# Optimization experiments

Hardware: AMD Instinct MI355X
Metric: run time of the kernel (lower is better)

Reference implementation:

```python
import jax, jax.numpy as jnp
import numpy as np

HEAD = 16
FEAT = 32
OUT = 32
N_E = 2048
N_UP = 1024  # n_up init kwarg (closed over; determines up/down split of x)


def _eps_ksi():
    # Complex-multiplication structure tensors (sparse 2x2x2), as in the source.
    ksi = (jnp.zeros((2, 2, 2))
           .at[0, 0, 0].set(1.0).at[1, 1, 0].set(-1.0)
           .at[0, 1, 1].set(1.0).at[1, 0, 1].set(1.0))
    eps = (jnp.zeros((2, 2, 2))
           .at[0, 0, 0].set(1.0).at[1, 1, 0].set(1.0)
           .at[0, 1, 1].set(1.0).at[1, 0, 1].set(-1.0))
    return eps, ksi


def setup_inputs() -> dict:
    key = jax.random.key(0)
    ks = jax.random.split(key, 9)
    x = jax.random.normal(ks[0], (N_E, FEAT, 3, 2), dtype=jnp.float32)
    # flax initializers.normal(1.0) -> stddev-1 normal params
    m_shape = (HEAD, FEAT, FEAT, 3, 2)
    a_shape = (HEAD, OUT, FEAT, 3, 2)
    return {
        'x': x,
        'M_uu': jax.random.normal(ks[1], m_shape, dtype=jnp.float32),
        'M_dd': jax.random.normal(ks[2], m_shape, dtype=jnp.float32),
        'M_ud': jax.random.normal(ks[3], m_shape, dtype=jnp.float32),
        'M_du': jax.random.normal(ks[4], m_shape, dtype=jnp.float32),
        'A_uu': jax.random.normal(ks[5], a_shape, dtype=jnp.float32),
        'A_dd': jax.random.normal(ks[6], a_shape, dtype=jnp.float32),
        'A_ud': jax.random.normal(ks[7], a_shape, dtype=jnp.float32),
        'A_du': jax.random.normal(ks[8], a_shape, dtype=jnp.float32),
    }


def reference(x, M_uu, M_dd, M_ud, M_du, A_uu, A_dd, A_ud, A_du):
    eps, ksi = _eps_ksi()
    u, d = x[:N_UP], x[N_UP:]  # up / down spin electrons

    def scores(q, k, M):
        # [h, n, m] attention logits, softmax over last axis (default in jax.nn.softmax)
        s = jnp.einsum('nfza,mgzb,hfgzc,abc->hnm', q, k, M, eps)
        return jax.nn.softmax(s)

    def combine(att, A, v):
        # [n, out_dims, 3, 2]
        return jnp.einsum('hnm,hgfza,mfzb,abc->ngzc', att, A, v, ksi)

    uu = scores(u, u, M_uu)
    dd = scores(d, d, M_dd)
    ud = scores(u, d, M_ud)
    du = scores(d, u, M_du)

    y_up = combine(uu, A_uu, u) + combine(ud, A_ud, d)
    y_dn = combine(dd, A_dd, d) + combine(du, A_du, u)
    return jnp.concatenate([y_up, y_dn], axis=0)  # [n_e, out_dims, 3, 2]
```

## Files before the change

### kernel.cpp

```cpp
#include <hip/hip_runtime.h>
#include <hip/hip_bf16.h>

typedef unsigned short u16;
typedef unsigned int   u32;
typedef _Float16 f16x8 __attribute__((ext_vector_type(8)));
typedef float    f32x16 __attribute__((ext_vector_type(16)));

#define HEADS 16
#define D     192
#define NUP   1024

#define XB       (2048ull*192*2)
#define XH_OFF   0ull
#define XL_OFF   (XH_OFF + XB)
#define XT_OFF   (XL_OFF + XB)
#define WM_BYTES (64ull*192*192*2)
#define WTP_OFF  (XT_OFF + XB)
#define MTH_OFF  (WTP_OFF + WM_BYTES)
#define MTL_OFF  (MTH_OFF + WM_BYTES)
#define Y_BYTES  (64ull*1024*192*2)
#define Y_OFF    (MTH_OFF + 2*WM_BYTES)
#define WS_NEED  (Y_OFF + Y_BYTES)

__device__ __forceinline__ u16 f2h(float v) {
    _Float16 h = (_Float16)v;
    return __builtin_bit_cast(u16, h);
}
__device__ __forceinline__ float h2f(u16 v) {
    return (float)__builtin_bit_cast(_Float16, v);
}
__device__ __forceinline__ u32 pk2h(float a, float b) {
    return (u32)f2h(a) | ((u32)f2h(b) << 16);
}
__device__ __forceinline__ u32 pk2h_rtz(float a, float b) {
    auto r = __builtin_amdgcn_cvt_pkrtz(a, b);
    return __builtin_bit_cast(u32, r);
}

__device__ __forceinline__ f16x8 make_bfrag(u32 q0, u32 q1, u32 q2, u32 q3, bool hi) {
    u32 s0 = (u32)__shfl_xor((int)q0, 32);
    u32 s1 = (u32)__shfl_xor((int)q1, 32);
    u32 s2 = (u32)__shfl_xor((int)q2, 32);
    u32 s3 = (u32)__shfl_xor((int)q3, 32);
    uint4 w;
    w.x = hi ? s2 : q0;  w.y = hi ? s3 : q1;
    w.z = hi ? q2 : s0;  w.w = hi ? q3 : s1;
    return __builtin_bit_cast(f16x8, w);
}

__global__ __launch_bounds__(512)
void prep_all(const float* __restrict__ x,
              const float* __restrict__ Muu, const float* __restrict__ Mdd,
              const float* __restrict__ Mud, const float* __restrict__ Mdu,
              const float* __restrict__ Auu, const float* __restrict__ Add,
              const float* __restrict__ Aud, const float* __restrict__ Adu,
              u16* __restrict__ xh, u16* __restrict__ xl, u16* __restrict__ xT,
              u16* __restrict__ wtp, u16* __restrict__ mth, u16* __restrict__ mtl)
{
    int b = blockIdx.x;
    if (b < 768) {
        int i = b*512 + threadIdx.x;
        float v = x[i];
        int n = i / D, d = i - n*D;
        u16 hi = f2h(v);
        xh[i] = hi;
        xl[i] = f2h(v - h2f(hi));
        xT[(size_t)(n >> 5)*6144 + d*32 + (n & 31)] = hi;
        return;
    }
    int idx = (b - 768)*512 + threadIdx.x;
    int th = idx / 36864, r = idx - th*36864;
    int dout = r / 192, din = r - dout*192;
    int t = th >> 4, h = th & 15;
    const float* Ap = (t==0)?Auu:(t==1)?Aud:(t==2)?Add:Adu;
    const float* Mp = (t==0)?Muu:(t==1)?Mud:(t==2)?Mdd:Mdu;
    int g = dout / 6, zc = dout - g*6, z = zc >> 1, b0 = zc & 1;
    int f = din / 6,  zb = din - f*6,  z2 = zb >> 1, b1 = zb & 1;

    float wv = 0.0f, mv = 0.0f;
    if (z2 == z) {
        const float* a = Ap + (((size_t)h*32 + g)*32 + f)*6 + z*2;
        float A0 = a[0], A1 = a[1];
        wv = (b0 == 0) ? (b1 == 0 ? A0 : -A1) : (b1 == 0 ? A1 : A0);
        const float* m = Mp + (((size_t)h*32 + f)*32 + g)*6 + z*2;
        float M0 = m[0], M1 = m[1];
        mv = (b0 == 0) ? (b1 == 0 ? M0 : -M1) : (b1 == 0 ? M1 : M0);
    }
    int ob = dout >> 5, l31 = dout & 31;
    int ks = din >> 4, kr = din & 15, g32 = kr >> 3, j = kr & 7;
    size_t pidx = ((((size_t)th*6 + ob)*12 + ks)*64 + g32*32 + l31)*8 + j;
    wtp[pidx] = f2h(wv);
    u16 mh = f2h(mv);
    mth[pidx] = mh;
    mtl[pidx] = f2h(mv - h2f(mh));
}

__global__ __launch_bounds__(512, 2)
void attn_mfma(const u16* __restrict__ xh_g,  const u16* __restrict__ xl_g,
               const u16* __restrict__ xT_g,  const u16* __restrict__ wtp_g,
               const u16* __restrict__ mth_g, const u16* __restrict__ mtl_g,
               u16* __restrict__ y_g)
{
    const int nt = blockIdx.x, h = blockIdx.y, t = blockIdx.z;
    const int tid  = threadIdx.x;
    const int lane = tid & 63;
    const int l31  = lane & 31;
    const int g32  = lane >> 5;
    const int th   = t*16 + h;
    const int n0   = nt*256 + (tid >> 6)*32;
    const int qoff = (t <= 1) ? 0 : NUP;
    const int koff = (t == 1 || t == 2) ? NUP : 0;
    const int mtb  = koff >> 5;

    __shared__ u16 sXh[3][32*200];
    __shared__ u16 sXT[3][192*40];

    f16x8 qh[12];
    {
        f16x8 bxh[12], bxl[12];
        const u16* xrh = xh_g + (size_t)(qoff + n0 + l31)*D;
        const u16* xrl = xl_g + (size_t)(qoff + n0 + l31)*D;
        #pragma unroll
        for (int ks = 0; ks < 12; ++ks) {
            bxh[ks] = *reinterpret_cast<const f16x8*>(xrh + ks*16 + g32*8);
            bxl[ks] = *reinterpret_cast<const f16x8*>(xrl + ks*16 + g32*8);
        }
        const u16* mthb = mth_g + (size_t)th*36864;
        const u16* mtlb = mtl_g + (size_t)th*36864;
        #pragma unroll
        for (int obp = 0; obp < 3; ++obp) {
            const int ob0 = obp*2, ob1 = obp*2 + 1;
            f32x16 a0, a1;
            #pragma unroll
            for (int i = 0; i < 16; ++i) { a0[i] = 0.0f; a1[i] = 0.0f; }
            #pragma unroll
            for (int ks = 0; ks < 12; ++ks) {
                size_t fo0 = (((size_t)ob0*12 + ks)*64 + lane)*8;
                size_t fo1 = (((size_t)ob1*12 + ks)*64 + lane)*8;
                f16x8 amh0 = *reinterpret_cast<const f16x8*>(mthb + fo0);
                f16x8 aml0 = *reinterpret_cast<const f16x8*>(mtlb + fo0);
                f16x8 amh1 = *reinterpret_cast<const f16x8*>(mthb + fo1);
                f16x8 aml1 = *reinterpret_cast<const f16x8*>(mtlb + fo1);
                a0 = __builtin_amdgcn_mfma_f32_32x32x16_f16(amh0, bxh[ks], a0, 0, 0, 0);
                a1 = __builtin_amdgcn_mfma_f32_32x32x16_f16(amh1, bxh[ks], a1, 0, 0, 0);
                a0 = __builtin_amdgcn_mfma_f32_32x32x16_f16(amh0, bxl[ks], a0, 0, 0, 0);
                a1 = __builtin_amdgcn_mfma_f32_32x32x16_f16(amh1, bxl[ks], a1, 0, 0, 0);
                a0 = __builtin_amdgcn_mfma_f32_32x32x16_f16(aml0, bxh[ks], a0, 0, 0, 0);
                a1 = __builtin_amdgcn_mfma_f32_32x32x16_f16(aml1, bxh[ks], a1, 0, 0, 0);
            }
            u32 h0[8], h1[8];
            #pragma unroll
            for (int j = 0; j < 8; ++j) {
                h0[j] = pk2h(a0[2*j], a0[2*j+1]);
                h1[j] = pk2h(a1[2*j], a1[2*j+1]);
            }
            qh[ob0*2+0] = make_bfrag(h0[0], h0[1], h0[2], h0[3], g32);
            qh[ob0*2+1] = make_bfrag(h0[4], h0[5], h0[6], h0[7], g32);
            qh[ob1*2+0] = make_bfrag(h1[0], h1[1], h1[2], h1[3], g32);
            qh[ob1*2+1] = make_bfrag(h1[4], h1[5], h1[6], h1[7], g32);
        }
    }

    f32x16 vt[6];
    #pragma unroll
    for (int ob = 0; ob < 6; ++ob)
        #pragma unroll
        for (int i = 0; i < 16; ++i) vt[ob][i] = 0.0f;

    float run_m = -3.0e38f, run_l = 0.0f;

    uint4 ld[3];
    auto load_tile = [&](int mt) {
        const int krow0 = koff + mt*32;
        #pragma unroll
        for (int i = 0; i < 3; ++i) {
            int c = tid + i*512;
            const u16* gp;
            if (c < 768) {
                int rr = c/24, cc = c - rr*24;
                gp = xh_g + (size_t)(krow0 + rr)*D + cc*8;
            } else {
                int c3 = c - 768, dd = c3 >> 2, qq = c3 & 3;
                gp = xT_g + (size_t)(mtb + mt)*6144 + dd*32 + qq*8;
            }
            ld[i] = *reinterpret_cast<const uint4*>(gp);
        }
    };
    auto store_tile = [&](int buf) {
        #pragma unroll
        for (int i = 0; i < 3; ++i) {
            int c = tid + i*512;
            u16* lp;
            if (c < 768) {
                int rr = c/24, cc = c - rr*24;  lp = &sXh[buf][rr*200 + cc*8];
            } else {
                int c3 = c - 768, dd = c3 >> 2, qq = c3 & 3;  lp = &sXT[buf][dd*40 + qq*8];
            }
            *reinterpret_cast<uint4*>(lp) = ld[i];
        }
    };
    auto SCORES = [&](int bc, f32x16 &sOut) {
        f32x16 s0, s1;
        #pragma unroll
        for (int i = 0; i < 16; ++i) { s0[i] = 0.0f; s1[i] = 0.0f; }
        __builtin_amdgcn_s_setprio(1);
        #pragma unroll
        for (int ks = 0; ks < 6; ++ks) {
            f16x8 ah0 = *reinterpret_cast<const f16x8*>(&sXh[bc][l31*200 + ks*16 + g32*8]);
            f16x8 ah1 = *reinterpret_cast<const f16x8*>(&sXh[bc][l31*200 + (ks+6)*16 + g32*8]);
            s0 = __builtin_amdgcn_mfma_f32_32x32x16_f16(ah0, qh[ks],   s0, 0, 0, 0);
            s1 = __builtin_amdgcn_mfma_f32_32x32x16_f16(ah1, qh[ks+6], s1, 0, 0, 0);
        }
        __builtin_amdgcn_s_setprio(0);
        #pragma unroll
        for (int i = 0; i < 16; ++i) sOut[i] = s0[i] + s1[i];
    };
    auto SOFTMAX = [&](f32x16 &sIn, f16x8 &pf0, f16x8 &pf1) {
        float tmax = sIn[0];
        #pragma unroll
        for (int i = 1; i < 16; ++i) tmax = fmaxf(tmax, sIn[i]);
        tmax = fmaxf(tmax, __shfl_xor(tmax, 32));
        if (__any(tmax > run_m + 8.0f)) {
            float nm = fmaxf(run_m, tmax);
            float rs = __expf(run_m - nm);
            #pragma unroll
            for (int ob = 0; ob < 6; ++ob)
                #pragma unroll
                for (int i = 0; i < 16; ++i) vt[ob][i] *= rs;
            run_l *= rs;
            run_m = nm;
        }
        float psum = 0.0f;
        u32 q[8];
        #pragma unroll
        for (int j = 0; j < 8; ++j) {
            float p0 = __expf(sIn[2*j]   - run_m);
            float p1 = __expf(sIn[2*j+1] - run_m);
            psum += p0 + p1;
            q[j] = pk2h_rtz(p0, p1);
        }
        psum += __shfl_xor(psum, 32);
        run_l += psum;
        pf0 = make_bfrag(q[0], q[1], q[2], q[3], g32);
        pf1 = make_bfrag(q[4], q[5], q[6], q[7], g32);
    };
    auto PV = [&](int bp, f16x8 pf0, f16x8 pf1) {
        __builtin_amdgcn_s_setprio(1);
        #pragma unroll
        for (int ob = 0; ob < 6; ++ob) {
            f16x8 a0 = *reinterpret_cast<const f16x8*>(&sXT[bp][(ob*32 + l31)*40 + g32*8]);
            f16x8 a1 = *reinterpret_cast<const f16x8*>(&sXT[bp][(ob*32 + l31)*40 + 16 + g32*8]);
            vt[ob] = __builtin_amdgcn_mfma_f32_32x32x16_f16(a0, pf0, vt[ob], 0, 0, 0);
            vt[ob] = __builtin_amdgcn_mfma_f32_32x32x16_f16(a1, pf1, vt[ob], 0, 0, 0);
        }
        __builtin_amdgcn_s_setprio(0);
    };

    f32x16 sA, sB;

    load_tile(0); store_tile(0); __syncthreads();
    load_tile(1);
    SCORES(0, sA);
    store_tile(1); __syncthreads();

    auto STEP = [&](int cur, f32x16 &sCur, f32x16 &sPrev, int bC, int bP, int bN) {
        if (cur < 31) load_tile(cur + 1);
        SCORES(bC, sCur);
        f16x8 pf0, pf1;
        SOFTMAX(sPrev, pf0, pf1);
        PV(bP, pf0, pf1);
        if (cur < 31) store_tile(bN);
        __syncthreads();
    };

    int b0 = 1, b1 = 0, b2 = 2;
    #pragma unroll 1
    for (int m2 = 1; m2 <= 29; m2 += 2) {
        STEP(m2,     sB, sA, b0, b1, b2);
        { int tq = b1; b1 = b0; b0 = b2; b2 = tq; }
        STEP(m2 + 1, sA, sB, b0, b1, b2);
        { int tq = b1; b1 = b0; b0 = b2; b2 = tq; }
    }
    STEP(31, sB, sA, b0, b1, b2);
    {
        f16x8 pf0, pf1;
        SOFTMAX(sB, pf0, pf1);
        PV(b0, pf0, pf1);
    }

    float inv = 1.0f / run_l;
    #pragma unroll
    for (int ob = 0; ob < 6; ++ob)
        #pragma unroll
        for (int i = 0; i < 16; ++i) vt[ob][i] *= inv;

    const u16* wbase = wtp_g + (size_t)th*36864;
    f32x16 y[6];
    #pragma unroll
    for (int ob = 0; ob < 6; ++ob)
        #pragma unroll
        for (int i = 0; i < 16; ++i) y[ob][i] = 0.0f;

    #pragma unroll
    for (int ob = 0; ob < 6; ++ob) {
        u32 qq[8];
        #pragma unroll
        for (int j = 0; j < 8; ++j) qq[j] = pk2h_rtz(vt[ob][2*j], vt[ob][2*j+1]);
        #pragma unroll
        for (int half = 0; half < 2; ++half) {
            int ks = ob*2 + half;
            f16x8 bfr = half ? make_bfrag(qq[4], qq[5], qq[6], qq[7], g32)
                             : make_bfrag(qq[0], qq[1], qq[2], qq[3], g32);
            #pragma unroll
            for (int ob2 = 0; ob2 < 6; ++ob2) {
                f16x8 a = *reinterpret_cast<const f16x8*>(
                    wbase + ((((size_t)ob2*12) + ks)*64 + lane)*8);
                y[ob2] = __builtin_amdgcn_mfma_f32_32x32x16_f16(a, bfr, y[ob2], 0, 0, 0);
            }
        }
    }

    u16* yrow = y_g + ((size_t)th*1024 + n0 + l31)*D;
    #pragma unroll
    for (int ob = 0; ob < 6; ++ob)
        #pragma unroll
        for (int rq = 0; rq < 4; ++rq) {
            uint2 v;
            v.x = pk2h_rtz(y[ob][rq*4+0], y[ob][rq*4+1]);
            v.y = pk2h_rtz(y[ob][rq*4+2], y[ob][rq*4+3]);
            *reinterpret_cast<uint2*>(yrow + ob*32 + rq*8 + g32*4) = v;
        }
}

__global__ __launch_bounds__(512)
void reduce_y(const u16* __restrict__ y_g, float* __restrict__ out)
{
    int gi = blockIdx.x*512 + threadIdx.x;
    int n = gi / 24, c = gi - n*24;
    int p = n >> 10, nn = n & 1023;
    float acc[8];
    #pragma unroll
    for (int j = 0; j < 8; ++j) acc[j] = 0.0f;
    #pragma unroll
    for (int k = 0; k < 32; ++k) {
        int tcur = p*2 + (k >> 4), hh = k & 15;
        uint4 v = *reinterpret_cast<const uint4*>(
            y_g + ((size_t)((tcur*16+hh)*1024 + nn))*D + c*8);
        u32 w[4] = {v.x, v.y, v.z, v.w};
        #pragma unroll
        for (int j = 0; j < 4; ++j) {
            acc[2*j]   += h2f((u16)(w[j] & 0xffffu));
            acc[2*j+1] += h2f((u16)(w[j] >> 16));
        }
    }
    float* op = out + (size_t)n*D + c*8;
    float4 o0 = {acc[0], acc[1], acc[2], acc[3]};
    float4 o1 = {acc[4], acc[5], acc[6], acc[7]};
    *reinterpret_cast<float4*>(op)     = o0;
    *reinterpret_cast<float4*>(op + 4) = o1;
}

__global__ __launch_bounds__(256, 2)
void attn_fused_fb(const float* __restrict__ x,
                const float* __restrict__ Muu, const float* __restrict__ Mdd,
                const float* __restrict__ Mud, const float* __restrict__ Mdu,
                const float* __restrict__ Auu, const float* __restrict__ Add,
                const float* __restrict__ Aud, const float* __restrict__ Adu,
                float* __restrict__ out)
{
    const int nt  = blockIdx.x;
    const int h   = blockIdx.y;
    const int t   = blockIdx.z;
    const int tid = threadIdx.x;
    const float* qb = (t <= 1) ? x : x + (size_t)NUP*D;
    const float* kb = (t == 0 || t == 3) ? x : x + (size_t)NUP*D;
    const float* Mp = (t==0)?Muu:(t==1)?Mud:(t==2)?Mdd:Mdu;
    const float* Ap = (t==0)?Auu:(t==1)?Aud:(t==2)?Add:Adu;
    const float* Mh = Mp + (size_t)h*32*D;
    const float* Ah = Ap + (size_t)h*32*D;
    float* ob = out + ((t>=2) ? (size_t)NUP*D : 0);

    __shared__ float sK[32*196];
    __shared__ float sQM[32*196];
    __shared__ float sS[32*33];
    __shared__ float sTmp[32*8];
    __shared__ float sR[32];
    __shared__ float sMaxRun[32];
    __shared__ float sSumRun[32];

    if (tid < 32) { sMaxRun[tid] = -3.0e38f; sSumRun[tid] = 0.0f; }
    for (int i = tid; i < 32*D/4; i += 256)
        reinterpret_cast<float4*>(sK)[i] = reinterpret_cast<const float4*>(Mh)[i];
    __syncthreads();

    #pragma unroll
    for (int kk = 0; kk < 4; ++kk) {
        int p = tid + kk*256;
        int n = p >> 5, g = p & 31;
        const float* qrow = qb + (size_t)(nt*32 + n)*D;
        float acc[6] = {0,0,0,0,0,0};
        for (int f = 0; f < 32; ++f) {
            const float* qf = qrow + f*6;
            const float* mf = sK + f*D + g*6;
            #pragma unroll
            for (int z = 0; z < 3; ++z) {
                float q0 = qf[2*z], q1 = qf[2*z+1];
                float m0 = mf[2*z], m1 = mf[2*z+1];
                acc[2*z]   += q0*m0 - q1*m1;
                acc[2*z+1] += q1*m0 + q0*m1;
            }
        }
        #pragma unroll
        for (int j = 0; j < 6; ++j) sQM[n*196 + g*6 + j] = acc[j];
    }

    const int gn = tid >> 5;
    const int cg = tid & 31;
    const int cbase = cg*6;
    float vacc[4][6];
    #pragma unroll
    for (int a = 0; a < 4; ++a)
        #pragma unroll
        for (int b = 0; b < 6; ++b) vacc[a][b] = 0.0f;

    const int txm = tid & 15, tyn = tid >> 4;

    for (int mt = 0; mt < 32; ++mt) {
        __syncthreads();
        for (int i = tid; i < 32*(D/4); i += 256) {
            int row = i / (D/4), j = i - row*(D/4);
            float4 v = reinterpret_cast<const float4*>(kb + (size_t)(mt*32 + row)*D)[j];
            *reinterpret_cast<float4*>(&sK[row*196 + j*4]) = v;
        }
        __syncthreads();

        float a00=0,a01=0,a10=0,a11=0;
        {
            const float* q0p = &sQM[tyn*196];
            const float* q1p = &sQM[(tyn+16)*196];
            const float* k0p = &sK[txm*196];
            const float* k1p = &sK[(txm+16)*196];
            for (int k = 0; k < D; k += 4) {
                float4 qa = *reinterpret_cast<const float4*>(q0p+k);
                float4 qc = *reinterpret_cast<const float4*>(q1p+k);
                float4 ka = *reinterpret_cast<const float4*>(k0p+k);
                float4 kc = *reinterpret_cast<const float4*>(k1p+k);
                a00 += qa.x*ka.x + qa.y*ka.y + qa.z*ka.z + qa.w*ka.w;
                a01 += qa.x*kc.x + qa.y*kc.y + qa.z*kc.z + qa.w*kc.w;
                a10 += qc.x*ka.x + qc.y*ka.y + qc.z*ka.z + qc.w*ka.w;
                a11 += qc.x*kc.x + qc.y*kc.y + qc.z*kc.z + qc.w*kc.w;
            }
        }
        sS[tyn*33 + txm]          = a00;
        sS[tyn*33 + txm+16]       = a01;
        sS[(tyn+16)*33 + txm]     = a10;
        sS[(tyn+16)*33 + txm+16]  = a11;
        __syncthreads();

        const int srow = tid >> 3, sj = tid & 7;
        {
            const float* r = &sS[srow*33];
            float mx = fmaxf(fmaxf(r[sj], r[sj+8]), fmaxf(r[sj+16], r[sj+24]));
            sTmp[srow*8 + sj] = mx;
        }
        __syncthreads();
        if (tid < 32) {
            float mx = sTmp[tid*8];
            #pragma unroll
            for (int j = 1; j < 8; ++j) mx = fmaxf(mx, sTmp[tid*8+j]);
            float om = sMaxRun[tid];
            float nm = fmaxf(om, mx);
            sR[tid] = __expf(om - nm);
            sMaxRun[tid] = nm;
        }
        __syncthreads();
        {
            float nm = sMaxRun[srow];
            float* r = &sS[srow*33];
            float p0 = __expf(r[sj]    - nm);
            float p1 = __expf(r[sj+8]  - nm);
            float p2 = __expf(r[sj+16] - nm);
            float p3 = __expf(r[sj+24] - nm);
            r[sj] = p0; r[sj+8] = p1; r[sj+16] = p2; r[sj+24] = p3;
            sTmp[srow*8+sj] = p0+p1+p2+p3;
        }
        __syncthreads();
        if (tid < 32) {
            float s = 0.0f;
            #pragma unroll
            for (int j = 0; j < 8; ++j) s += sTmp[tid*8+j];
            sSumRun[tid] = sSumRun[tid]*sR[tid] + s;
        }
        {
            float r0 = sR[gn*4+0], r1 = sR[gn*4+1], r2 = sR[gn*4+2], r3 = sR[gn*4+3];
            #pragma unroll
            for (int b = 0; b < 6; ++b) { vacc[0][b]*=r0; vacc[1][b]*=r1; vacc[2][b]*=r2; vacc[3][b]*=r3; }
            for (int m = 0; m < 32; ++m) {
                float p0 = sS[(gn*4+0)*33+m];
                float p1 = sS[(gn*4+1)*33+m];
                float p2 = sS[(gn*4+2)*33+m];
                float p3 = sS[(gn*4+3)*33+m];
                const float* kr = &sK[m*196 + cbase];
                #pragma unroll
                for (int b = 0; b < 6; ++b) {
                    float kv = kr[b];
                    vacc[0][b] += p0*kv;
                    vacc[1][b] += p1*kv;
                    vacc[2][b] += p2*kv;
                    vacc[3][b] += p3*kv;
                }
            }
        }
    }

    __syncthreads();
    {
        float i0 = 1.0f/sSumRun[gn*4+0], i1 = 1.0f/sSumRun[gn*4+1];
        float i2 = 1.0f/sSumRun[gn*4+2], i3 = 1.0f/sSumRun[gn*4+3];
        #pragma unroll
        for (int b = 0; b < 6; ++b) {
            sQM[(gn*4+0)*196 + cbase + b] = vacc[0][b]*i0;
            sQM[(gn*4+1)*196 + cbase + b] = vacc[1][b]*i1;
            sQM[(gn*4+2)*196 + cbase + b] = vacc[2][b]*i2;
            sQM[(gn*4+3)*196 + cbase + b] = vacc[3][b]*i3;
        }
    }
    for (int i = tid; i < 32*D/4; i += 256)
        reinterpret_cast<float4*>(sK)[i] = reinterpret_cast<const float4*>(Ah)[i];
    __syncthreads();

    #pragma unroll
    for (int kk = 0; kk < 4; ++kk) {
        int p = tid + kk*256;
        int n = p >> 5, g = p & 31;
        float acc[6] = {0,0,0,0,0,0};
        const float* vb = &sQM[n*196];
        const float* ab = &sK[g*D];
        for (int f = 0; f < 32; ++f) {
            const float* vf = vb + f*6;
            const float* af = ab + f*6;
            #pragma unroll
            for (int z = 0; z < 3; ++z) {
                float V0 = vf[2*z], V1 = vf[2*z+1];
                float A0 = af[2*z], A1 = af[2*z+1];
                acc[2*z]   += A0*V0 - A1*V1;
                acc[2*z+1] += A0*V1 + A1*V0;
            }
        }
        float* op = ob + (size_t)(nt*32 + n)*D + g*6;
        #pragma unroll
        for (int j = 0; j < 6; ++j) atomicAdd(op + j, acc[j]);
    }
}

extern "C" void kernel_launch(void* const* d_in, const int* in_sizes, int n_in,
                              void* d_out, int out_size, void* d_ws, size_t ws_size,
                              hipStream_t stream) {
    const float* x   = (const float*)d_in[0];
    const float* Muu = (const float*)d_in[1];
    const float* Mdd = (const float*)d_in[2];
    const float* Mud = (const float*)d_in[3];
    const float* Mdu = (const float*)d_in[4];
    const float* Auu = (const float*)d_in[5];
    const float* Add = (const float*)d_in[6];
    const float* Aud = (const float*)d_in[7];
    const float* Adu = (const float*)d_in[8];
    float* outp = (float*)d_out;

    if (ws_size >= WS_NEED) {
        char* ws = (char*)d_ws;
        u16* xh  = (u16*)(ws + XH_OFF);
        u16* xl  = (u16*)(ws + XL_OFF);
        u16* xT  = (u16*)(ws + XT_OFF);
        u16* wtp = (u16*)(ws + WTP_OFF);
        u16* mth = (u16*)(ws + MTH_OFF);
        u16* mtl = (u16*)(ws + MTL_OFF);
        u16* y   = (u16*)(ws + Y_OFF);

        prep_all<<<5376, 512, 0, stream>>>(x, Muu, Mdd, Mud, Mdu,
                                           Auu, Add, Aud, Adu,
                                           xh, xl, xT, wtp, mth, mtl);
        attn_mfma<<<dim3(4, 16, 4), 512, 0, stream>>>(xh, xl, xT, wtp, mth, mtl, y);
        reduce_y<<<96, 512, 0, stream>>>(y, outp);
    } else {
        (void)hipMemsetAsync(d_out, 0, (size_t)out_size * sizeof(float), stream);
        attn_fused_fb<<<dim3(32, 16, 4), 256, 0, stream>>>(x, Muu, Mdd, Mud, Mdu,
                                                           Auu, Add, Aud, Adu, outp);
    }
}
```

Baseline: 128.2 us.

## Halve attention block size and shrink LDS buffering to raise occupancy

Each attention block now runs 256 threads (4 waves, 128 query rows) instead of 512, and the grid doubles in x to keep the same total work. The LDS ring shrinks from triple-buffered K and V^T tiles to a single K tile plus double-buffered V^T. The lower per-block LDS footprint and smaller blocks are meant to fit more blocks per CU and give the scheduler more independent work. In exchange, each K tile is loaded from global memory by twice as many blocks, and the single K buffer needs an extra __syncthreads per step before the next tile is stored.

```diff
diff --git a/kernel.cpp b/kernel.cpp
--- a/kernel.cpp
+++ b/kernel.cpp
@@ -95,7 +95,7 @@
     mtl[pidx] = f2h(mv - h2f(mh));
 }
 
-__global__ __launch_bounds__(512, 2)
+__global__ __launch_bounds__(256, 2)
 void attn_mfma(const u16* __restrict__ xh_g,  const u16* __restrict__ xl_g,
                const u16* __restrict__ xT_g,  const u16* __restrict__ wtp_g,
                const u16* __restrict__ mth_g, const u16* __restrict__ mtl_g,
@@ -107,13 +107,13 @@
     const int l31  = lane & 31;
     const int g32  = lane >> 5;
     const int th   = t*16 + h;
-    const int n0   = nt*256 + (tid >> 6)*32;
+    const int n0   = nt*128 + (tid >> 6)*32;
     const int qoff = (t <= 1) ? 0 : NUP;
     const int koff = (t == 1 || t == 2) ? NUP : 0;
     const int mtb  = koff >> 5;
 
-    __shared__ u16 sXh[3][32*200];
-    __shared__ u16 sXT[3][192*40];
+    __shared__ u16 sXh[32*200];
+    __shared__ u16 sXT[2][192*40];
 
     f16x8 qh[12];
     {
@@ -169,12 +169,12 @@
 
     float run_m = -3.0e38f, run_l = 0.0f;
 
-    uint4 ld[3];
+    uint4 ld[6];
     auto load_tile = [&](int mt) {
         const int krow0 = koff + mt*32;
         #pragma unroll
-        for (int i = 0; i < 3; ++i) {
-            int c = tid + i*512;
+        for (int i = 0; i < 6; ++i) {
+            int c = tid + i*256;
             const u16* gp;
             if (c < 768) {
                 int rr = c/24, cc = c - rr*24;
@@ -186,28 +186,28 @@
             ld[i] = *reinterpret_cast<const uint4*>(gp);
         }
     };
-    auto store_tile = [&](int buf) {
-        #pragma unroll
-        for (int i = 0; i < 3; ++i) {
-            int c = tid + i*512;
+    auto store_tile = [&](int xb) {
+        #pragma unroll
+        for (int i = 0; i < 6; ++i) {
+            int c = tid + i*256;
             u16* lp;
             if (c < 768) {
-                int rr = c/24, cc = c - rr*24;  lp = &sXh[buf][rr*200 + cc*8];
+                int rr = c/24, cc = c - rr*24;  lp = &sXh[rr*200 + cc*8];
             } else {
-                int c3 = c - 768, dd = c3 >> 2, qq = c3 & 3;  lp = &sXT[buf][dd*40 + qq*8];
+                int c3 = c - 768, dd = c3 >> 2, qq = c3 & 3;  lp = &sXT[xb][dd*40 + qq*8];
             }
             *reinterpret_cast<uint4*>(lp) = ld[i];
         }
     };
-    auto SCORES = [&](int bc, f32x16 &sOut) {
+    auto SCORES = [&](f32x16 &sOut) {
         f32x16 s0, s1;
         #pragma unroll
         for (int i = 0; i < 16; ++i) { s0[i] = 0.0f; s1[i] = 0.0f; }
         __builtin_amdgcn_s_setprio(1);
         #pragma unroll
         for (int ks = 0; ks < 6; ++ks) {
-            f16x8 ah0 = *reinterpret_cast<const f16x8*>(&sXh[bc][l31*200 + ks*16 + g32*8]);
-            f16x8 ah1 = *reinterpret_cast<const f16x8*>(&sXh[bc][l31*200 + (ks+6)*16 + g32*8]);
+            f16x8 ah0 = *reinterpret_cast<const f16x8*>(&sXh[l31*200 + ks*16 + g32*8]);
+            f16x8 ah1 = *reinterpret_cast<const f16x8*>(&sXh[l31*200 + (ks+6)*16 + g32*8]);
             s0 = __builtin_amdgcn_mfma_f32_32x32x16_f16(ah0, qh[ks],   s0, 0, 0, 0);
             s1 = __builtin_amdgcn_mfma_f32_32x32x16_f16(ah1, qh[ks+6], s1, 0, 0, 0);
         }
@@ -260,32 +260,34 @@
 
     load_tile(0); store_tile(0); __syncthreads();
     load_tile(1);
-    SCORES(0, sA);
-    store_tile(1); __syncthreads();
-
-    auto STEP = [&](int cur, f32x16 &sCur, f32x16 &sPrev, int bC, int bP, int bN) {
+    SCORES(sA);
+    __syncthreads();
+    store_tile(1);
+    __syncthreads();
+
+    auto STEP = [&](int cur, f32x16 &sCur, f32x16 &sPrev) {
         if (cur < 31) load_tile(cur + 1);
-        SCORES(bC, sCur);
+        SCORES(sCur);
         f16x8 pf0, pf1;
         SOFTMAX(sPrev, pf0, pf1);
-        PV(bP, pf0, pf1);
-        if (cur < 31) store_tile(bN);
-        __syncthreads();
+        PV((cur - 1) & 1, pf0, pf1);
+        __syncthreads();
+        if (cur < 31) {
+            store_tile((cur + 1) & 1);
+            __syncthreads();
+        }
     };
 
-    int b0 = 1, b1 = 0, b2 = 2;
     #pragma unroll 1
     for (int m2 = 1; m2 <= 29; m2 += 2) {
-        STEP(m2,     sB, sA, b0, b1, b2);
-        { int tq = b1; b1 = b0; b0 = b2; b2 = tq; }
-        STEP(m2 + 1, sA, sB, b0, b1, b2);
-        { int tq = b1; b1 = b0; b0 = b2; b2 = tq; }
-    }
-    STEP(31, sB, sA, b0, b1, b2);
+        STEP(m2,     sB, sA);
+        STEP(m2 + 1, sA, sB);
+    }
+    STEP(31, sB, sA);
     {
         f16x8 pf0, pf1;
         SOFTMAX(sB, pf0, pf1);
-        PV(b0, pf0, pf1);
+        PV(1, pf0, pf1);
     }
 
     float inv = 1.0f / run_l;
@@ -580,7 +582,7 @@
         prep_all<<<5376, 512, 0, stream>>>(x, Muu, Mdd, Mud, Mdu,
                                            Auu, Add, Aud, Adu,
                                            xh, xl, xT, wtp, mth, mtl);
-        attn_mfma<<<dim3(4, 16, 4), 512, 0, stream>>>(xh, xl, xT, wtp, mth, mtl, y);
+        attn_mfma<<<dim3(8, 16, 4), 256, 0, stream>>>(xh, xl, xT, wtp, mth, mtl, y);
         reduce_y<<<96, 512, 0, stream>>>(y, outp);
     } else {
         (void)hipMemsetAsync(d_out, 0, (size_t)out_size * sizeof(float), stream);
```

New measurement: 170.8 us. 33.3% more time.
